# Kernel tuning notes

Measured on AMD Instinct MI355X. Metric: run time of the kernel, lower is better.

Reference implementation:

```python
import jax, jax.numpy as jnp
import numpy as np

SQ2PI = 0.79788456
M, D_IN, H1, H2, D_OUT = 256, 784, 256, 256, 10


def setup_inputs() -> dict:
    key = jax.random.key(0)
    ks = jax.random.split(key, 6)
    x = jax.random.normal(ks[0], (M, D_IN), dtype=jnp.float32)
    target = jax.random.randint(ks[1], (M,), 0, D_OUT)

    def init_w(k, fan_in, fan_out):
        # torch init: uniform(-1/sqrt(size(1)), 1/sqrt(size(1))) * scale (scale=1)
        stdv = 1.0 / np.sqrt(fan_out)
        return jax.random.uniform(k, (fan_in, fan_out), jnp.float32, -stdv, stdv)

    w0 = init_w(ks[2], D_IN, H1)
    w1 = init_w(ks[3], H1, H2)
    w2 = init_w(ks[4], H2, H2)
    wlast = init_w(ks[5], H2, D_OUT)
    th0 = jnp.zeros((1, H1), jnp.float32)
    th1 = jnp.zeros((1, H2), jnp.float32)
    th2 = jnp.zeros((1, H2), jnp.float32)
    thlast = jnp.zeros((1, D_OUT), jnp.float32)
    return dict(x=x, target=target, w0=w0, w1=w1, w2=w2, wlast=wlast,
                th0=th0, th1=th1, th2=th2, thlast=thlast)


def _mvg_layer(xbar, xcov, m, th):
    # sigma[b] = m^T @ xcov[b] @ m + diag(sum_j 1 - m[j,:]^2)
    s = jnp.sum(1.0 - m ** 2, axis=0)                      # [H2]
    t = jnp.einsum('bjk,kl->bjl', xcov, m)                 # [B,H,H2]
    sigma = jnp.einsum('ji,bjl->bil', m, t) + jnp.diag(s)[None]  # [B,H2,H2]
    diagsig = jnp.diagonal(sigma, axis1=1, axis2=2)        # [B,H2]
    hbar = xbar @ m + th                                   # [B,H2]
    xbar_next = jnp.tanh(SQ2PI * hbar / jnp.sqrt(diagsig))
    c = (1.0 - xbar_next ** 2) / jnp.sqrt(diagsig)         # [B,H2]
    eye = jnp.eye(m.shape[1], dtype=xbar.dtype)
    xcov_next = (SQ2PI * sigma * c[:, :, None] * c[:, None, :]
                 + eye[None] * (1.0 - xbar_next[:, None, :] ** 2))
    return xbar_next, xcov_next


def reference(x, target, w0, w1, w2, wlast, th0, th1, th2, thlast):
    m0 = 2.0 * jax.nn.sigmoid(w0) - 1.0
    m1 = 2.0 * jax.nn.sigmoid(w1) - 1.0
    m2 = 2.0 * jax.nn.sigmoid(w2) - 1.0
    mlast = 2.0 * jax.nn.sigmoid(wlast) - 1.0

    # first layer: xcov for input is implicitly zero, sigma is diagonal
    diagsig1 = jnp.sum(1.0 - m0 ** 2, axis=0)              # [H1]
    h1bar = x @ m0 + th0                                   # [M,H1]
    x1bar = jnp.tanh(SQ2PI * h1bar / jnp.sqrt(diagsig1))
    eye1 = jnp.eye(m0.shape[1], dtype=x.dtype)
    xcov1 = eye1[None] * (1.0 - x1bar[:, None, :] ** 2)    # [M,H1,H1]

    x2bar, xcov2 = _mvg_layer(x1bar, xcov1, m1, th1)
    x3bar, xcov3 = _mvg_layer(x2bar, xcov2, m2, th2)

    hlastbar = x3bar @ mlast + thlast                      # [M,10]
    logprobs = jax.nn.log_softmax(hlastbar, axis=-1)
    loss = -jnp.mean(jnp.take_along_axis(logprobs, target[:, None], axis=1))
    pred = jnp.argmax(hlastbar, axis=1)
    frac_correct = jnp.mean((pred == target).astype(jnp.float32))
    return (hlastbar, logprobs, xcov3, loss, frac_correct)
```

## Files before the change

### kernel.cpp

```cpp
#include <hip/hip_runtime.h>
#include <hip/hip_fp8.h>
#include <math.h>

#define SQ2PI_F 0.79788456f

typedef __attribute__((ext_vector_type(4))) float f32x4;
typedef __attribute__((address_space(1))) unsigned int gas_u32;
typedef __attribute__((address_space(3))) unsigned int las_u32;

__device__ inline unsigned short bf16rne(float x) {
  unsigned int u = __float_as_uint(x);
  u += 0x7fffu + ((u >> 16) & 1u);
  return (unsigned short)(u >> 16);
}
__device__ inline unsigned char f2fp8(float v) { return __hip_fp8_e4m3(v).__x; }
__device__ inline float fp8tof(unsigned char b) {
  __hip_fp8_e4m3 h;
  h.__x = (__hip_fp8_storage_t)b;
  return (float)h;
}
__device__ inline unsigned int pk_fp8x4(f32x4 v) {
  return (unsigned int)f2fp8(v[0]) | ((unsigned int)f2fp8(v[1]) << 8) |
         ((unsigned int)f2fp8(v[2]) << 16) | ((unsigned int)f2fp8(v[3]) << 24);
}

__global__ void k_prep(const float* __restrict__ w0, const float* __restrict__ w1,
                       const float* __restrict__ w2, const float* __restrict__ wlast,
                       float* __restrict__ m0, float* __restrict__ m1,
                       unsigned char* __restrict__ m1f8t, float* __restrict__ m2,
                       unsigned char* __restrict__ m2f8, float* __restrict__ mlast,
                       float* __restrict__ lf) {
  int b = blockIdx.x, t = threadIdx.x;
  if (b < 784) {
    int i = b * 256 + t;
    m0[i] = tanhf(0.5f * w0[i]);
  } else if (b < 1040) {
    int j = b - 784;
    float v = tanhf(0.5f * w1[j * 256 + t]);
    m1[j * 256 + t] = v;
    m1f8t[t * 256 + j] = f2fp8(v);
  } else if (b < 1296) {
    int j = b - 1040;
    float v = tanhf(0.5f * w2[j * 256 + t]);
    m2[j * 256 + t] = v;
    m2f8[t * 256 + j] = f2fp8(v);
  } else {
    int i = (b - 1296) * 256 + t;
    if (i < 2560) mlast[i] = tanhf(0.5f * wlast[i]);
    if (b == 1296 && t < 2) lf[t] = 0.f;
  }
}

__global__ void k_layer1(const float* __restrict__ x, const float* __restrict__ m0,
                         const float* __restrict__ th0,
                         float* __restrict__ x1bar, float* __restrict__ d1) {
  __shared__ float xr[784];
  __shared__ float ph[256], pd[256];
  int r = blockIdx.x, t = threadIdx.x;
  int j = t & 255, h = t >> 8;
  for (int p = t; p < 784; p += 512) xr[p] = x[r * 784 + p];
  __syncthreads();
  float acch = 0.f, accd = 0.f;
  int k0 = h * 392, k1 = k0 + 392;
#pragma unroll 8
  for (int k = k0; k < k1; ++k) {
    float mm = m0[k * 256 + j];
    acch = fmaf(xr[k], mm, acch);
    accd = fmaf(-mm, mm, accd + 1.f);
  }
  if (h) { ph[j] = acch; pd[j] = accd; }
  __syncthreads();
  if (!h) {
    acch += ph[j];
    accd += pd[j];
    float rs = rsqrtf(accd);
    float xb = tanhf(SQ2PI_F * (acch + th0[j]) * rs);
    x1bar[r * 256 + j] = xb;
    d1[r * 256 + j] = 1.f - xb * xb;
  }
}

__global__ void k_layer2(const float* __restrict__ d1, const float* __restrict__ x1bar,
                         const float* __restrict__ m1, const float* __restrict__ m2,
                         const float* __restrict__ th1, const float* __restrict__ th2,
                         float* __restrict__ c2, float* __restrict__ d2p,
                         float* __restrict__ h3bar,
                         float* __restrict__ s1g, float* __restrict__ s2g) {
  __shared__ float pd[256], ph[256], ps[256], sx[256], p3[256], q2[256];
  int r = blockIdx.x, t = threadIdx.x;
  int i = t & 255, h = t >> 8;
  int j0 = h * 128, j1 = j0 + 128;
  float accd = 0.f, acch = 0.f, accs = 0.f;
  for (int j = j0; j < j1; ++j) {
    float mm = m1[j * 256 + i];
    accd = fmaf(d1[r * 256 + j] * mm, mm, accd);
    acch = fmaf(x1bar[r * 256 + j], mm, acch);
    accs = fmaf(-mm, mm, accs + 1.f);
  }
  if (h) { pd[i] = accd; ph[i] = acch; ps[i] = accs; }
  __syncthreads();
  if (!h) {
    accd += pd[i];
    acch += ph[i];
    accs += ps[i];
    float rs = rsqrtf(accd + accs);
    float xb = tanhf(SQ2PI_F * (acch + th1[i]) * rs);
    float d = 1.f - xb * xb;
    c2[r * 256 + i] = d * rs;
    d2p[r * 256 + i] = d;
    sx[i] = xb;
    if (r == 0) s1g[i] = accs;
  }
  __syncthreads();
  float acc3 = 0.f, acc2 = 0.f;
  for (int j = j0; j < j1; ++j) {
    float mm = m2[j * 256 + i];
    acc3 = fmaf(sx[j], mm, acc3);
    acc2 = fmaf(-mm, mm, acc2 + 1.f);
  }
  if (h) { p3[i] = acc3; q2[i] = acc2; }
  __syncthreads();
  if (!h) {
    h3bar[r * 256 + i] = acc3 + p3[i] + th2[i];
    if (r == 0) s2g[i] = acc2 + q2[i];
  }
}

__global__ __launch_bounds__(1024, 4) void k_fused(
    const unsigned char* __restrict__ m1f8t, const unsigned char* __restrict__ m2f8,
    const float* __restrict__ d1, const float* __restrict__ c2,
    const float* __restrict__ d2p, const float* __restrict__ s1,
    const float* __restrict__ s2, const float* __restrict__ h3bar,
    float* __restrict__ x3bar, float* __restrict__ xcov3) {
  __shared__ __align__(16) unsigned char XC[67584];
  __shared__ __align__(16) unsigned char SB[2][16384];
  __shared__ __align__(16) unsigned char XB[2][16384];
  __shared__ float c2L[256], d2pL[256], s1L[256], s2L[256];
  __shared__ float dsig[256], c3L[256], d3L[256];

  const int b = blockIdx.x;
  const int tid = threadIdx.x;
  const int l = tid & 63, w = tid >> 6;
  const int lr = l & 15, lk = l >> 4;
  const int R = w * 16;

  auto stage_f8 = [&](const unsigned char* gsrc, unsigned char* sb) {
    int rl = w * 4 + (l >> 4);
    int c = l & 15;
    const unsigned char* src = gsrc + rl * 256 + ((c ^ (rl & 7)) << 4);
    unsigned char* dst = sb + w * 1024;
    __builtin_amdgcn_global_load_lds((const gas_u32*)src, (las_u32*)dst, 16, 0, 0);
  };

#define PRD8(S, p, kc) \
  (*(const long*)((const unsigned char*)(S) + ((p) << 8) + ((((kc) ^ (((p) & 7) << 1))) << 3)))

  stage_f8(m1f8t, SB[0]);

  if (tid < 256) {
    c2L[tid] = c2[b * 256 + tid];
    d2pL[tid] = d2p[b * 256 + tid];
    s1L[tid] = s1[tid];
    s2L[tid] = s2[tid];
    dsig[tid] = 0.f;
  }

  const float* d1b = d1 + b * 256;

  long af_w[8];
#pragma unroll
  for (int ks = 0; ks < 8; ++ks) {
    unsigned long long mr =
        *(const unsigned long long*)(m1f8t + (size_t)(R + lr) * 256 + ks * 32 + lk * 8);
    const float* dp = d1b + ks * 32 + lk * 8;
    unsigned long long out = 0;
#pragma unroll
    for (int e = 0; e < 8; ++e) {
      float v = fp8tof((unsigned char)(mr >> (8 * e))) * dp[e];
      out |= ((unsigned long long)f2fp8(v)) << (8 * e);
    }
    af_w[ks] = (long)out;
  }
  __syncthreads();

  long afX[8];

#pragma unroll
  for (int cp = 0; cp < 4; ++cp) {
    if (cp < 3)
      stage_f8(m1f8t + (size_t)(cp + 1) * 16384, SB[(cp + 1) & 1]);
    else
      stage_f8(m2f8, SB[0]);
    const unsigned char* sbc = SB[cp & 1];
    f32x4 acc[4];
#pragma unroll
    for (int j = 0; j < 4; ++j) acc[j] = {0.f, 0.f, 0.f, 0.f};
#pragma unroll
    for (int ks = 0; ks < 8; ++ks) {
#pragma unroll
      for (int j = 0; j < 4; ++j) {
        long bq = PRD8(sbc, j * 16 + lr, ks * 4 + lk);
        acc[j] = __builtin_amdgcn_mfma_f32_16x16x32_fp8_fp8(af_w[ks], bq, acc[j], 0, 0, 0);
      }
    }
    unsigned char* XP = XB[cp & 1];
    int r0 = R + lk * 4;
#pragma unroll
    for (int j = 0; j < 4; ++j) {
      int p = j * 16 + lr;
      int cc = cp * 64 + p;
      float c2c = c2L[cc];
      f32x4 st;
#pragma unroll
      for (int e = 0; e < 4; ++e) {
        int r = r0 + e;
        float g = acc[j][e];
        if (r == cc) g += s1L[r];
        float v = SQ2PI_F * c2L[r] * c2c * g;
        if (r == cc) v += d2pL[r];
        st[e] = v;
      }
      *(unsigned int*)(XP + (p << 8) + ((((r0 >> 3) ^ ((p & 7) << 1))) << 3) + (r0 & 7)) =
          pk_fp8x4(st);
    }
    __syncthreads();
    if (cp == (w >> 2)) {
      int p2 = (w & 3) * 16 + lr;
#pragma unroll
      for (int ks = 0; ks < 8; ++ks) afX[ks] = PRD8(XP, p2, ks * 4 + lk);
    }
  }

#pragma unroll
  for (int lp = 0; lp < 4; ++lp) {
    if (lp < 3) stage_f8(m2f8 + (size_t)(lp + 1) * 16384, SB[(lp + 1) & 1]);
    const unsigned char* sbt = SB[lp & 1];
    f32x4 at[4];
#pragma unroll
    for (int j = 0; j < 4; ++j) at[j] = {0.f, 0.f, 0.f, 0.f};
#pragma unroll
    for (int ks = 0; ks < 8; ++ks) {
#pragma unroll
      for (int j = 0; j < 4; ++j) {
        long bq = PRD8(sbt, j * 16 + lr, ks * 4 + lk);
        at[j] = __builtin_amdgcn_mfma_f32_16x16x32_fp8_fp8(afX[ks], bq, at[j], 0, 0, 0);
      }
    }
    int j0 = R + lk * 4;
#pragma unroll
    for (int jf = 0; jf < 4; ++jf) {
      int p = jf * 16 + lr;
      int lq = lp * 64 + p;
      *(unsigned int*)(XC + (size_t)lq * 264 + j0) = pk_fp8x4(at[jf]);
      unsigned int mraw = *(const unsigned int*)(
          sbt + (p << 8) + ((((j0 >> 3) ^ ((p & 7) << 1))) << 3) + (j0 & 7));
      float s = 0.f;
#pragma unroll
      for (int e = 0; e < 4; ++e)
        s = fmaf(fp8tof((unsigned char)(mraw >> (8 * e))), at[jf][e], s);
      s += __shfl_xor(s, 16, 64);
      s += __shfl_xor(s, 32, 64);
      if (lk == 0) atomicAdd(&dsig[lq], s);
    }
    __syncthreads();
  }

  if (tid < 256) {
    float ds = dsig[tid] + s2L[tid];
    float rs = rsqrtf(ds);
    float xb = tanhf(SQ2PI_F * h3bar[b * 256 + tid] * rs);
    x3bar[b * 256 + tid] = xb;
    float d = 1.f - xb * xb;
    c3L[tid] = d * rs;
    d3L[tid] = d;
  }
  __syncthreads();

  long am2[8];
#pragma unroll
  for (int ks = 0; ks < 8; ++ks)
    am2[ks] = *(const long*)(m2f8 + (size_t)(R + lr) * 256 + ks * 32 + lk * 8);

#pragma unroll
  for (int lp = 0; lp < 4; ++lp) {
    f32x4 sc[4];
#pragma unroll
    for (int j = 0; j < 4; ++j) sc[j] = {0.f, 0.f, 0.f, 0.f};
#pragma unroll
    for (int ks = 0; ks < 8; ++ks) {
#pragma unroll
      for (int j = 0; j < 4; ++j) {
        int p = lp * 64 + j * 16 + lr;
        long bq = *(const long*)(XC + (size_t)p * 264 + (ks * 4 + lk) * 8);
        sc[j] = __builtin_amdgcn_mfma_f32_16x16x32_fp8_fp8(am2[ks], bq, sc[j], 0, 0, 0);
      }
    }
    int i0 = R + lk * 4;
#pragma unroll
    for (int lf = 0; lf < 4; ++lf) {
      int gl = lp * 64 + lf * 16 + lr;
      float cg = c3L[gl];
      f32x4 st;
#pragma unroll
      for (int e = 0; e < 4; ++e) {
        int i = i0 + e;
        float g = sc[lf][e];
        if (i == gl) g += s2L[i];
        float v = SQ2PI_F * c3L[i] * cg * g;
        if (i == gl) v += d3L[i];
        st[e] = v;
      }
      *(f32x4*)(xcov3 + ((size_t)b << 16) + (size_t)gl * 256 + i0) = st;
    }
  }
#undef PRD8
}

__global__ void k_final4(const float* __restrict__ x3bar, const float* __restrict__ mlast,
                         const float* __restrict__ thlast, const int* __restrict__ target,
                         float* __restrict__ hlast_out, float* __restrict__ logp_out,
                         float* __restrict__ loss_out, float* __restrict__ frac_out) {
  __shared__ float Wl[2560];
  int t = threadIdx.x;
  int r = blockIdx.x * 64 + t;
  for (int p = t; p < 2560; p += 64) Wl[p] = mlast[p];
  __syncthreads();
  float acc[10];
#pragma unroll
  for (int c = 0; c < 10; ++c) acc[c] = thlast[c];
  for (int j = 0; j < 256; ++j) {
    float xv = x3bar[r * 256 + j];
#pragma unroll
    for (int c = 0; c < 10; ++c) acc[c] = fmaf(xv, Wl[j * 10 + c], acc[c]);
  }
#pragma unroll
  for (int c = 0; c < 10; ++c) hlast_out[r * 10 + c] = acc[c];
  float mx = acc[0];
  int am = 0;
#pragma unroll
  for (int c = 1; c < 10; ++c)
    if (acc[c] > mx) { mx = acc[c]; am = c; }
  float se = 0.f;
#pragma unroll
  for (int c = 0; c < 10; ++c) se += expf(acc[c] - mx);
  float lse = logf(se);
#pragma unroll
  for (int c = 0; c < 10; ++c) logp_out[r * 10 + c] = acc[c] - mx - lse;
  int tg = target[r];
  float lossc = -(acc[tg] - mx - lse) * (1.f / 256.f);
  float corr = (am == tg) ? (1.f / 256.f) : 0.f;
#pragma unroll
  for (int off = 32; off > 0; off >>= 1) {
    lossc += __shfl_down(lossc, off);
    corr += __shfl_down(corr, off);
  }
  if (t == 0) {
    atomicAdd(loss_out, lossc);
    atomicAdd(frac_out, corr);
  }
}


extern "C" void kernel_launch(void* const* d_in, const int* in_sizes, int n_in,
                              void* d_out, int out_size, void* d_ws, size_t ws_size,
                              hipStream_t stream) {
  const float* x = (const float*)d_in[0];
  const int* target = (const int*)d_in[1];
  const float* w0 = (const float*)d_in[2];
  const float* w1 = (const float*)d_in[3];
  const float* w2 = (const float*)d_in[4];
  const float* wlast = (const float*)d_in[5];
  const float* th0 = (const float*)d_in[6];
  const float* th1 = (const float*)d_in[7];
  const float* th2 = (const float*)d_in[8];
  const float* thlast = (const float*)d_in[9];

  float* W = (float*)d_ws;
  size_t o = 0;
  auto alloc = [&](size_t n) { float* p = W + o; o += n; return p; };
  float* m0 = alloc(200704);
  float* m1 = alloc(65536);
  float* m2 = alloc(65536);
  float* mlast = alloc(2560);
  float* s1 = alloc(256);
  float* s2 = alloc(256);
  float* x1bar = alloc(65536);
  float* d1 = alloc(65536);
  float* c2 = alloc(65536);
  float* d2p = alloc(65536);
  float* h3bar = alloc(65536);
  float* x3bar = alloc(65536);
  unsigned char* m1f8t = (unsigned char*)alloc(16384);
  unsigned char* m2f8 = (unsigned char*)alloc(16384);

  float* hlast = (float*)d_out;
  float* logp = hlast + 2560;
  float* xcov3_out = logp + 2560;
  float* loss = xcov3_out + 16777216;
  float* frac = loss + 1;

  k_prep<<<1306, 256, 0, stream>>>(w0, w1, w2, wlast, m0, m1, m1f8t, m2, m2f8,
                                   mlast, loss);
  k_layer1<<<256, 512, 0, stream>>>(x, m0, th0, x1bar, d1);
  k_layer2<<<256, 512, 0, stream>>>(d1, x1bar, m1, m2, th1, th2, c2, d2p,
                                    h3bar, s1, s2);
  k_fused<<<256, 1024, 0, stream>>>(m1f8t, m2f8, d1, c2, d2p, s1, s2,
                                    h3bar, x3bar, xcov3_out);
  k_final4<<<4, 64, 0, stream>>>(x3bar, mlast, thlast, target, hlast, logp, loss, frac);
}
```

Before: 135.0 us.

## Fuse layer1/layer2 kernels and keep m2 resident in LDS in fused covariance kernel

Merges the first two small per-row kernels into one, so x1bar and d1 stay in shared memory and one launch plus a global round trip are dropped. In the main fused kernel, the whole fp8 m2 matrix is loaded once into LDS instead of being streamed in chunks. The intermediate products are stored with the same swizzle instead of a padded layout, and the m1 staging chunks are halved. This removes repeated global staging and several barriers in the second and third GEMM phases. The cost is higher LDS usage, which may limit occupancy, and more loop iterations in the first phase.

```diff
diff --git a/kernel.cpp b/kernel.cpp
--- a/kernel.cpp
+++ b/kernel.cpp
@@ -8,11 +8,6 @@
 typedef __attribute__((address_space(1))) unsigned int gas_u32;
 typedef __attribute__((address_space(3))) unsigned int las_u32;
 
-__device__ inline unsigned short bf16rne(float x) {
-  unsigned int u = __float_as_uint(x);
-  u += 0x7fffu + ((u >> 16) & 1u);
-  return (unsigned short)(u >> 16);
-}
 __device__ inline unsigned char f2fp8(float v) { return __hip_fp8_e4m3(v).__x; }
 __device__ inline float fp8tof(unsigned char b) {
   __hip_fp8_e4m3 h;
@@ -51,78 +46,82 @@
   }
 }
 
-__global__ void k_layer1(const float* __restrict__ x, const float* __restrict__ m0,
-                         const float* __restrict__ th0,
-                         float* __restrict__ x1bar, float* __restrict__ d1) {
+__global__ void k_layers(const float* __restrict__ x, const float* __restrict__ m0,
+                         const float* __restrict__ m1, const float* __restrict__ m2,
+                         const float* __restrict__ th0, const float* __restrict__ th1,
+                         const float* __restrict__ th2,
+                         float* __restrict__ d1g, float* __restrict__ c2,
+                         float* __restrict__ d2p, float* __restrict__ h3bar,
+                         float* __restrict__ s1g, float* __restrict__ s2g) {
   __shared__ float xr[784];
-  __shared__ float ph[256], pd[256];
-  int r = blockIdx.x, t = threadIdx.x;
-  int j = t & 255, h = t >> 8;
-  for (int p = t; p < 784; p += 512) xr[p] = x[r * 784 + p];
-  __syncthreads();
-  float acch = 0.f, accd = 0.f;
-  int k0 = h * 392, k1 = k0 + 392;
-#pragma unroll 8
-  for (int k = k0; k < k1; ++k) {
-    float mm = m0[k * 256 + j];
-    acch = fmaf(xr[k], mm, acch);
-    accd = fmaf(-mm, mm, accd + 1.f);
-  }
-  if (h) { ph[j] = acch; pd[j] = accd; }
-  __syncthreads();
-  if (!h) {
-    acch += ph[j];
-    accd += pd[j];
-    float rs = rsqrtf(accd);
-    float xb = tanhf(SQ2PI_F * (acch + th0[j]) * rs);
-    x1bar[r * 256 + j] = xb;
-    d1[r * 256 + j] = 1.f - xb * xb;
-  }
-}
-
-__global__ void k_layer2(const float* __restrict__ d1, const float* __restrict__ x1bar,
-                         const float* __restrict__ m1, const float* __restrict__ m2,
-                         const float* __restrict__ th1, const float* __restrict__ th2,
-                         float* __restrict__ c2, float* __restrict__ d2p,
-                         float* __restrict__ h3bar,
-                         float* __restrict__ s1g, float* __restrict__ s2g) {
-  __shared__ float pd[256], ph[256], ps[256], sx[256], p3[256], q2[256];
+  __shared__ float pa[256], pb[256], pc[256];
+  __shared__ float sx1[256], sd1[256], sx2[256];
   int r = blockIdx.x, t = threadIdx.x;
   int i = t & 255, h = t >> 8;
-  int j0 = h * 128, j1 = j0 + 128;
-  float accd = 0.f, acch = 0.f, accs = 0.f;
-  for (int j = j0; j < j1; ++j) {
-    float mm = m1[j * 256 + i];
-    accd = fmaf(d1[r * 256 + j] * mm, mm, accd);
-    acch = fmaf(x1bar[r * 256 + j], mm, acch);
-    accs = fmaf(-mm, mm, accs + 1.f);
-  }
-  if (h) { pd[i] = accd; ph[i] = acch; ps[i] = accs; }
-  __syncthreads();
-  if (!h) {
-    accd += pd[i];
-    acch += ph[i];
-    accs += ps[i];
-    float rs = rsqrtf(accd + accs);
-    float xb = tanhf(SQ2PI_F * (acch + th1[i]) * rs);
-    float d = 1.f - xb * xb;
-    c2[r * 256 + i] = d * rs;
-    d2p[r * 256 + i] = d;
-    sx[i] = xb;
-    if (r == 0) s1g[i] = accs;
-  }
-  __syncthreads();
-  float acc3 = 0.f, acc2 = 0.f;
-  for (int j = j0; j < j1; ++j) {
-    float mm = m2[j * 256 + i];
-    acc3 = fmaf(sx[j], mm, acc3);
-    acc2 = fmaf(-mm, mm, acc2 + 1.f);
-  }
-  if (h) { p3[i] = acc3; q2[i] = acc2; }
-  __syncthreads();
-  if (!h) {
-    h3bar[r * 256 + i] = acc3 + p3[i] + th2[i];
-    if (r == 0) s2g[i] = acc2 + q2[i];
+  for (int p = t; p < 784; p += 512) xr[p] = x[r * 784 + p];
+  __syncthreads();
+  {
+    float acch = 0.f, accd = 0.f;
+    int k0 = h * 392, k1 = k0 + 392;
+#pragma unroll 8
+    for (int k = k0; k < k1; ++k) {
+      float mm = m0[k * 256 + i];
+      acch = fmaf(xr[k], mm, acch);
+      accd = fmaf(-mm, mm, accd + 1.f);
+    }
+    if (h) { pa[i] = acch; pb[i] = accd; }
+    __syncthreads();
+    if (!h) {
+      acch += pa[i];
+      accd += pb[i];
+      float rs = rsqrtf(accd);
+      float xb = tanhf(SQ2PI_F * (acch + th0[i]) * rs);
+      float d = 1.f - xb * xb;
+      sx1[i] = xb;
+      sd1[i] = d;
+      d1g[r * 256 + i] = d;
+    }
+    __syncthreads();
+  }
+  {
+    float accd = 0.f, acch = 0.f, accs = 0.f;
+    int j0 = h * 128, j1 = j0 + 128;
+    for (int j = j0; j < j1; ++j) {
+      float mm = m1[j * 256 + i];
+      accd = fmaf(sd1[j] * mm, mm, accd);
+      acch = fmaf(sx1[j], mm, acch);
+      accs = fmaf(-mm, mm, accs + 1.f);
+    }
+    if (h) { pa[i] = accd; pb[i] = acch; pc[i] = accs; }
+    __syncthreads();
+    if (!h) {
+      accd += pa[i];
+      acch += pb[i];
+      accs += pc[i];
+      float rs = rsqrtf(accd + accs);
+      float xb = tanhf(SQ2PI_F * (acch + th1[i]) * rs);
+      float d = 1.f - xb * xb;
+      c2[r * 256 + i] = d * rs;
+      d2p[r * 256 + i] = d;
+      sx2[i] = xb;
+      if (r == 0) s1g[i] = accs;
+    }
+    __syncthreads();
+  }
+  {
+    float acc3 = 0.f, acc2 = 0.f;
+    int j0 = h * 128, j1 = j0 + 128;
+    for (int j = j0; j < j1; ++j) {
+      float mm = m2[j * 256 + i];
+      acc3 = fmaf(sx2[j], mm, acc3);
+      acc2 = fmaf(-mm, mm, acc2 + 1.f);
+    }
+    if (h) { pa[i] = acc3; pb[i] = acc2; }
+    __syncthreads();
+    if (!h) {
+      h3bar[r * 256 + i] = acc3 + pa[i] + th2[i];
+      if (r == 0) s2g[i] = acc2 + pb[i];
+    }
   }
 }
 
@@ -132,9 +131,9 @@
     const float* __restrict__ d2p, const float* __restrict__ s1,
     const float* __restrict__ s2, const float* __restrict__ h3bar,
     float* __restrict__ x3bar, float* __restrict__ xcov3) {
-  __shared__ __align__(16) unsigned char XC[67584];
-  __shared__ __align__(16) unsigned char SB[2][16384];
-  __shared__ __align__(16) unsigned char XB[2][16384];
+  __shared__ __align__(16) unsigned char m2L[65536];
+  __shared__ __align__(16) unsigned char XC[65536];
+  __shared__ __align__(16) unsigned char SB[2][8192];
   __shared__ float c2L[256], d2pL[256], s1L[256], s2L[256];
   __shared__ float dsig[256], c3L[256], d3L[256];
 
@@ -144,18 +143,25 @@
   const int lr = l & 15, lk = l >> 4;
   const int R = w * 16;
 
-  auto stage_f8 = [&](const unsigned char* gsrc, unsigned char* sb) {
+#define PRD8(S, p, kc) \
+  (*(const long*)((const unsigned char*)(S) + ((p) << 8) + ((((kc) ^ (((p) & 7) << 1))) << 3)))
+#define SWZ32(p, j0) (((p) << 8) + ((((j0) >> 3) ^ (((p) & 7) << 1)) << 3) + ((j0) & 7))
+
+#pragma unroll
+  for (int q = 0; q < 4; ++q) {
+    int rl = q * 64 + w * 4 + (l >> 4);
+    int c = l & 15;
+    const unsigned char* src = m2f8 + rl * 256 + ((c ^ (rl & 7)) << 4);
+    unsigned char* dst = m2L + (q * 64 + w * 4) * 256;
+    __builtin_amdgcn_global_load_lds((const gas_u32*)src, (las_u32*)dst, 16, 0, 0);
+  }
+  if (w < 8) {
     int rl = w * 4 + (l >> 4);
     int c = l & 15;
-    const unsigned char* src = gsrc + rl * 256 + ((c ^ (rl & 7)) << 4);
-    unsigned char* dst = sb + w * 1024;
-    __builtin_amdgcn_global_load_lds((const gas_u32*)src, (las_u32*)dst, 16, 0, 0);
-  };
-
-#define PRD8(S, p, kc) \
-  (*(const long*)((const unsigned char*)(S) + ((p) << 8) + ((((kc) ^ (((p) & 7) << 1))) << 3)))
-
-  stage_f8(m1f8t, SB[0]);
+    const unsigned char* src = m1f8t + rl * 256 + ((c ^ (rl & 7)) << 4);
+    __builtin_amdgcn_global_load_lds((const gas_u32*)src,
+                                     (las_u32*)(SB[0] + (w * 4) * 256), 16, 0, 0);
+  }
 
   if (tid < 256) {
     c2L[tid] = c2[b * 256 + tid];
@@ -186,29 +192,32 @@
   long afX[8];
 
 #pragma unroll
-  for (int cp = 0; cp < 4; ++cp) {
-    if (cp < 3)
-      stage_f8(m1f8t + (size_t)(cp + 1) * 16384, SB[(cp + 1) & 1]);
-    else
-      stage_f8(m2f8, SB[0]);
+  for (int cp = 0; cp < 8; ++cp) {
+    if (cp < 7 && w < 8) {
+      int rl = w * 4 + (l >> 4);
+      int c = l & 15;
+      const unsigned char* src =
+          m1f8t + (size_t)(cp + 1) * 8192 + rl * 256 + ((c ^ (rl & 7)) << 4);
+      __builtin_amdgcn_global_load_lds(
+          (const gas_u32*)src, (las_u32*)(SB[(cp + 1) & 1] + (w * 4) * 256), 16, 0, 0);
+    }
     const unsigned char* sbc = SB[cp & 1];
-    f32x4 acc[4];
-#pragma unroll
-    for (int j = 0; j < 4; ++j) acc[j] = {0.f, 0.f, 0.f, 0.f};
+    f32x4 acc[2];
+    acc[0] = {0.f, 0.f, 0.f, 0.f};
+    acc[1] = {0.f, 0.f, 0.f, 0.f};
 #pragma unroll
     for (int ks = 0; ks < 8; ++ks) {
-#pragma unroll
-      for (int j = 0; j < 4; ++j) {
-        long bq = PRD8(sbc, j * 16 + lr, ks * 4 + lk);
-        acc[j] = __builtin_amdgcn_mfma_f32_16x16x32_fp8_fp8(af_w[ks], bq, acc[j], 0, 0, 0);
-      }
-    }
-    unsigned char* XP = XB[cp & 1];
+      long bq0 = PRD8(sbc, lr, ks * 4 + lk);
+      long bq1 = PRD8(sbc, 16 + lr, ks * 4 + lk);
+      acc[0] = __builtin_amdgcn_mfma_f32_16x16x32_fp8_fp8(af_w[ks], bq0, acc[0], 0, 0, 0);
+      acc[1] = __builtin_amdgcn_mfma_f32_16x16x32_fp8_fp8(af_w[ks], bq1, acc[1], 0, 0, 0);
+    }
+    unsigned char* XP = XC + (cp & 1) * 8192;
     int r0 = R + lk * 4;
 #pragma unroll
-    for (int j = 0; j < 4; ++j) {
+    for (int j = 0; j < 2; ++j) {
       int p = j * 16 + lr;
-      int cc = cp * 64 + p;
+      int cc = cp * 32 + p;
       float c2c = c2L[cc];
       f32x4 st;
 #pragma unroll
@@ -220,50 +229,38 @@
         if (r == cc) v += d2pL[r];
         st[e] = v;
       }
-      *(unsigned int*)(XP + (p << 8) + ((((r0 >> 3) ^ ((p & 7) << 1))) << 3) + (r0 & 7)) =
-          pk_fp8x4(st);
-    }
-    __syncthreads();
-    if (cp == (w >> 2)) {
-      int p2 = (w & 3) * 16 + lr;
+      *(unsigned int*)(XP + SWZ32(p, r0)) = pk_fp8x4(st);
+    }
+    __syncthreads();
+    if (cp == (w >> 1)) {
+      int p2 = (w & 1) * 16 + lr;
 #pragma unroll
       for (int ks = 0; ks < 8; ++ks) afX[ks] = PRD8(XP, p2, ks * 4 + lk);
     }
   }
-
-#pragma unroll
-  for (int lp = 0; lp < 4; ++lp) {
-    if (lp < 3) stage_f8(m2f8 + (size_t)(lp + 1) * 16384, SB[(lp + 1) & 1]);
-    const unsigned char* sbt = SB[lp & 1];
-    f32x4 at[4];
-#pragma unroll
-    for (int j = 0; j < 4; ++j) at[j] = {0.f, 0.f, 0.f, 0.f};
+  __syncthreads();
+
+#pragma unroll
+  for (int lf = 0; lf < 16; ++lf) {
+    f32x4 at = {0.f, 0.f, 0.f, 0.f};
 #pragma unroll
     for (int ks = 0; ks < 8; ++ks) {
-#pragma unroll
-      for (int j = 0; j < 4; ++j) {
-        long bq = PRD8(sbt, j * 16 + lr, ks * 4 + lk);
-        at[j] = __builtin_amdgcn_mfma_f32_16x16x32_fp8_fp8(afX[ks], bq, at[j], 0, 0, 0);
-      }
+      long bq = PRD8(m2L, lf * 16 + lr, ks * 4 + lk);
+      at = __builtin_amdgcn_mfma_f32_16x16x32_fp8_fp8(afX[ks], bq, at, 0, 0, 0);
     }
     int j0 = R + lk * 4;
-#pragma unroll
-    for (int jf = 0; jf < 4; ++jf) {
-      int p = jf * 16 + lr;
-      int lq = lp * 64 + p;
-      *(unsigned int*)(XC + (size_t)lq * 264 + j0) = pk_fp8x4(at[jf]);
-      unsigned int mraw = *(const unsigned int*)(
-          sbt + (p << 8) + ((((j0 >> 3) ^ ((p & 7) << 1))) << 3) + (j0 & 7));
-      float s = 0.f;
-#pragma unroll
-      for (int e = 0; e < 4; ++e)
-        s = fmaf(fp8tof((unsigned char)(mraw >> (8 * e))), at[jf][e], s);
-      s += __shfl_xor(s, 16, 64);
-      s += __shfl_xor(s, 32, 64);
-      if (lk == 0) atomicAdd(&dsig[lq], s);
-    }
-    __syncthreads();
-  }
+    int lq = lf * 16 + lr;
+    *(unsigned int*)(XC + SWZ32(lq, j0)) = pk_fp8x4(at);
+    unsigned int mraw = *(const unsigned int*)(m2L + SWZ32(lq, j0));
+    float s = 0.f;
+#pragma unroll
+    for (int e = 0; e < 4; ++e)
+      s = fmaf(fp8tof((unsigned char)(mraw >> (8 * e))), at[e], s);
+    s += __shfl_xor(s, 16, 64);
+    s += __shfl_xor(s, 32, 64);
+    if (lk == 0) atomicAdd(&dsig[lq], s);
+  }
+  __syncthreads();
 
   if (tid < 256) {
     float ds = dsig[tid] + s2L[tid];
@@ -278,42 +275,34 @@
 
   long am2[8];
 #pragma unroll
-  for (int ks = 0; ks < 8; ++ks)
-    am2[ks] = *(const long*)(m2f8 + (size_t)(R + lr) * 256 + ks * 32 + lk * 8);
-
-#pragma unroll
-  for (int lp = 0; lp < 4; ++lp) {
-    f32x4 sc[4];
-#pragma unroll
-    for (int j = 0; j < 4; ++j) sc[j] = {0.f, 0.f, 0.f, 0.f};
+  for (int ks = 0; ks < 8; ++ks) am2[ks] = PRD8(m2L, R + lr, ks * 4 + lk);
+
+#pragma unroll
+  for (int lf = 0; lf < 16; ++lf) {
+    f32x4 sc = {0.f, 0.f, 0.f, 0.f};
+    int p = lf * 16 + lr;
 #pragma unroll
     for (int ks = 0; ks < 8; ++ks) {
-#pragma unroll
-      for (int j = 0; j < 4; ++j) {
-        int p = lp * 64 + j * 16 + lr;
-        long bq = *(const long*)(XC + (size_t)p * 264 + (ks * 4 + lk) * 8);
-        sc[j] = __builtin_amdgcn_mfma_f32_16x16x32_fp8_fp8(am2[ks], bq, sc[j], 0, 0, 0);
-      }
+      long bq = PRD8(XC, p, ks * 4 + lk);
+      sc = __builtin_amdgcn_mfma_f32_16x16x32_fp8_fp8(am2[ks], bq, sc, 0, 0, 0);
     }
     int i0 = R + lk * 4;
-#pragma unroll
-    for (int lf = 0; lf < 4; ++lf) {
-      int gl = lp * 64 + lf * 16 + lr;
-      float cg = c3L[gl];
-      f32x4 st;
-#pragma unroll
-      for (int e = 0; e < 4; ++e) {
-        int i = i0 + e;
-        float g = sc[lf][e];
-        if (i == gl) g += s2L[i];
-        float v = SQ2PI_F * c3L[i] * cg * g;
-        if (i == gl) v += d3L[i];
-        st[e] = v;
-      }
-      *(f32x4*)(xcov3 + ((size_t)b << 16) + (size_t)gl * 256 + i0) = st;
-    }
+    int gl = p;
+    float cg = c3L[gl];
+    f32x4 st;
+#pragma unroll
+    for (int e = 0; e < 4; ++e) {
+      int i = i0 + e;
+      float g = sc[e];
+      if (i == gl) g += s2L[i];
+      float v = SQ2PI_F * c3L[i] * cg * g;
+      if (i == gl) v += d3L[i];
+      st[e] = v;
+    }
+    *(f32x4*)(xcov3 + ((size_t)b << 16) + (size_t)gl * 256 + i0) = st;
   }
 #undef PRD8
+#undef SWZ32
 }
 
 __global__ void k_final4(const float* __restrict__ x3bar, const float* __restrict__ mlast,
@@ -384,7 +373,6 @@
   float* mlast = alloc(2560);
   float* s1 = alloc(256);
   float* s2 = alloc(256);
-  float* x1bar = alloc(65536);
   float* d1 = alloc(65536);
   float* c2 = alloc(65536);
   float* d2p = alloc(65536);
@@ -401,8 +389,7 @@
 
   k_prep<<<1306, 256, 0, stream>>>(w0, w1, w2, wlast, m0, m1, m1f8t, m2, m2f8,
                                    mlast, loss);
-  k_layer1<<<256, 512, 0, stream>>>(x, m0, th0, x1bar, d1);
-  k_layer2<<<256, 512, 0, stream>>>(d1, x1bar, m1, m2, th1, th2, c2, d2p,
+  k_layers<<<256, 512, 0, stream>>>(x, m0, m1, m2, th0, th1, th2, d1, c2, d2p,
                                     h3bar, s1, s2);
   k_fused<<<256, 1024, 0, stream>>>(m1f8t, m2f8, d1, c2, d2p, s1, s2,
                                     h3bar, x3bar, xcov3_out);
```

Result: faster. 129.4 us (-4.1%).
